# Kernel tuning notes

Measured on AMD Instinct MI355X. Metric: run time of the kernel, lower is better.

Reference implementation:

```python
import jax, jax.numpy as jnp
import numpy as np

S = 1    # support_num
K = 20   # KNN neighbor count for conv layers
B, V = 4, 4096


def _normalize(x, axis):
    n = jnp.linalg.norm(x, axis=axis, keepdims=True)
    return x / jnp.maximum(n, 1e-12)


def _knn(v, k):
    # v: (b, n, 3) -> (b, n, k) indices of k nearest (excluding self)
    sq = jnp.sum(v * v, axis=-1)
    dist = sq[:, :, None] + sq[:, None, :] - 2.0 * jnp.einsum('bic,bjc->bij', v, v)
    return jax.lax.top_k(-dist, k + 1)[1][:, :, 1:]


def _gather(feat, idx):
    # feat (b,n,c), idx (b,n,k) -> (b,n,k,c)
    return feat[jnp.arange(feat.shape[0])[:, None, None], idx]


def _dir_norm(verts, idx):
    nb = _gather(verts, idx)                       # (b,v,k,3)
    return _normalize(nb - verts[:, :, None, :], -1)


def _conv_surface(idx, verts, directions, kernel_num):
    b, v, k = idx.shape
    nd = _dir_norm(verts, idx)
    sd = _normalize(directions, 0)                 # (3, S*kernel_num)
    theta = jax.nn.relu(jnp.einsum('bvkc,cm->bvkm', nd, sd))
    theta = theta.reshape(b, v, k, S, kernel_num)
    return jnp.sum(jnp.max(theta, axis=2), axis=2)  # (b,v,kernel_num)


def _conv_layer(idx, verts, fm, W, bias, directions, out_c):
    b, v, k = idx.shape
    nd = _dir_norm(verts, idx)
    sd = _normalize(directions, 0)                 # (3, S*out_c)
    theta = jax.nn.relu(jnp.einsum('bvkc,cm->bvkm', nd, sd))  # (b,v,k,S*out_c)
    fo = fm @ W + bias                             # (b,v,(S+1)*out_c)
    center = fo[:, :, :out_c]
    support = _gather(fo[:, :, out_c:], idx)       # (b,v,k,S*out_c)
    act = (theta * support).reshape(b, v, k, S, out_c)
    return center + jnp.sum(jnp.max(act, axis=2), axis=2)


def _pool(verts, fm, rate, nn, seed):
    b, v, _ = verts.shape
    idx = _knn(verts, nn)
    pooled = jnp.max(_gather(fm, idx), axis=2)
    sel = jax.random.permutation(jax.random.key(seed), v)[: v // rate]
    return verts[:, sel, :], pooled[:, sel, :]


def _ln(x, g, b):
    m = jnp.mean(x, -1, keepdims=True)
    var = jnp.mean(jnp.square(x - m), -1, keepdims=True)
    return (x - m) / jnp.sqrt(var + 1e-6) * g + b


def _mha(q, kv, Win, bin_, Wout, bout, h):
    E = q.shape[-1]
    hd = E // h
    wq, wk, wv = jnp.split(Win, 3, axis=0)
    bq, bk, bv = jnp.split(bin_, 3)

    def heads(x, w, bb_):
        y = x @ w.T + bb_
        return y.reshape(y.shape[0], y.shape[1], h, hd).transpose(0, 2, 1, 3)

    qh, kh, vh = heads(q, wq, bq), heads(kv, wk, bk), heads(kv, wv, bv)
    a = jax.nn.softmax(jnp.einsum('bhqd,bhkd->bhqk', qh, kh) / jnp.sqrt(jnp.float32(hd)), -1)
    o = jnp.einsum('bhqk,bhkd->bhqd', a, vh).transpose(0, 2, 1, 3).reshape(q.shape)
    return o @ Wout.T + bout


def _conv1x1(x, W, b):
    # x (B,C,N,1) -> (B,O,N,1)
    return jnp.einsum('bcnl,oc->bonl', x, W) + b[None, :, None, None]


def _bn_train(x, g, b):
    # BatchNorm2d in training mode (batch statistics), eps=1e-5
    m = jnp.mean(x, axis=(0, 2, 3), keepdims=True)
    v = jnp.var(x, axis=(0, 2, 3), keepdims=True)
    return (x - m) / jnp.sqrt(v + 1e-5) * g[None, :, None, None] + b[None, :, None, None]


def _forward(vertices, d0, g0, be0, w1, b1, dir1, g1, be1, w2, b2, dir2, g2, be2,
             w3, b3, dir3, g3, be3, token, a1_in_w, a1_in_b, a1_out_w, a1_out_b,
             ffn1_w, ffn1_b, bg, bb, ffn2_w, ffn2_b, a2_in_w, a2_in_b, a2_out_w,
             a2_out_b, w7, b7, dir7, g4, be4, c8_w, c8_b):
    b = vertices.shape[0]
    v0 = vertices[:, 0]                                 # (b, 4096, 3)
    idx0 = _knn(v0, K)
    fm0 = jax.nn.relu(_ln(_conv_surface(idx0, v0, d0, 32), g0, be0))
    fm1 = jax.nn.relu(_ln(_conv_layer(idx0, v0, fm0, w1, b1, dir1, 64), g1, be1))
    v1, fm1 = _pool(v0, fm1, 4, 4, 1)                   # (b,1024,3), (b,1024,64)
    idx1 = _knn(v1, K)
    fm_x = fm1
    fm2 = jax.nn.relu(_ln(_conv_layer(idx1, v1, fm1, w2, b2, dir2, 128), g2, be2))
    fm3 = jax.nn.relu(_ln(_conv_layer(idx1, v1, fm2, w3, b3, dir3, 256), g3, be3))
    _, fm3 = _pool(v1, fm3, 4, 4, 2)                    # (b,256,256)
    tok = jnp.tile(token, (b, 1, 1, 1))[:, :, :, 0].transpose(0, 2, 1)  # (b,1024,64)
    query = _mha(tok, fm_x, a1_in_w, a1_in_b, a1_out_w, a1_out_b, 4) + fm_x
    q2 = query.transpose(0, 2, 1)[:, :, :, None]        # (b,64,1024,1)
    q2 = _conv1x1(jax.nn.relu(_bn_train(_conv1x1(q2, ffn1_w, ffn1_b), bg, bb)), ffn2_w, ffn2_b)
    query = q2[:, :, :, 0].transpose(0, 2, 1)           # (b,1024,256)
    cross = _mha(query, fm3, a2_in_w, a2_in_b, a2_out_w, a2_out_b, 4) + query
    fmf = jax.nn.relu(_ln(_conv_layer(idx1, v1, cross, w7, b7, dir7, 1024), g4, be4))
    fmf = fmf.transpose(0, 2, 1)[:, :, :, None]         # (b,1024,1024,1)
    return _conv1x1(fmf, c8_w, c8_b)                    # (b,256,1024,1)


def setup_inputs():
    ks = iter(jax.random.split(jax.random.key(0), 64))

    def rn(shape, s=0.05):
        return jax.random.normal(next(ks), shape, dtype=jnp.float32) * s

    f32 = jnp.float32
    return dict(
        vertices=jax.random.normal(next(ks), (B, 1, V, 3), dtype=f32),
        d0=rn((3, S * 32)), g0=jnp.ones((32,), f32), be0=jnp.zeros((32,), f32),
        w1=rn((32, (S + 1) * 64)), b1=rn(((S + 1) * 64,)), dir1=rn((3, S * 64)),
        g1=jnp.ones((64,), f32), be1=jnp.zeros((64,), f32),
        w2=rn((64, (S + 1) * 128)), b2=rn(((S + 1) * 128,)), dir2=rn((3, S * 128)),
        g2=jnp.ones((128,), f32), be2=jnp.zeros((128,), f32),
        w3=rn((128, (S + 1) * 256)), b3=rn(((S + 1) * 256,)), dir3=rn((3, S * 256)),
        g3=jnp.ones((256,), f32), be3=jnp.zeros((256,), f32),
        token=rn((1, 64, 1024, 1), 1.0),
        a1_in_w=rn((192, 64)), a1_in_b=rn((192,)), a1_out_w=rn((64, 64)), a1_out_b=rn((64,)),
        ffn1_w=rn((256, 64)), ffn1_b=rn((256,)), bg=jnp.ones((256,), f32), bb=jnp.zeros((256,), f32),
        ffn2_w=rn((256, 256)), ffn2_b=rn((256,)),
        a2_in_w=rn((768, 256)), a2_in_b=rn((768,)), a2_out_w=rn((256, 256)), a2_out_b=rn((256,)),
        w7=rn((256, (S + 1) * 1024)), b7=rn(((S + 1) * 1024,)), dir7=rn((3, S * 1024)),
        g4=jnp.ones((1024,), f32), be4=jnp.zeros((1024,), f32),
        c8_w=rn((256, 1024)), c8_b=rn((256,)),
    )


def reference(vertices, d0, g0, be0, w1, b1, dir1, g1, be1, w2, b2, dir2, g2, be2,
              w3, b3, dir3, g3, be3, token, a1_in_w, a1_in_b, a1_out_w, a1_out_b,
              ffn1_w, ffn1_b, bg, bb, ffn2_w, ffn2_b, a2_in_w, a2_in_b, a2_out_w,
              a2_out_b, w7, b7, dir7, g4, be4, c8_w, c8_b):
    return _forward(vertices, d0, g0, be0, w1, b1, dir1, g1, be1, w2, b2, dir2, g2,
                    be2, w3, b3, dir3, g3, be3, token, a1_in_w, a1_in_b, a1_out_w,
                    a1_out_b, ffn1_w, ffn1_b, bg, bb, ffn2_w, ffn2_b, a2_in_w,
                    a2_in_b, a2_out_w, a2_out_b, w7, b7, dir7, g4, be4, c8_w, c8_b)
```

## Files before the change

kernel.cpp:

```cpp
#include <hip/hip_runtime.h>
#include <stdint.h>
#include <stddef.h>

#define FINF __builtin_inff()

__device__ inline void tf2x32(uint32_t k0, uint32_t k1, uint32_t x0, uint32_t x1,
                              uint32_t* o0, uint32_t* o1) {
  uint32_t ks2 = k0 ^ k1 ^ 0x1BD11BDAu;
  uint32_t v0 = x0 + k0, v1 = x1 + k1;
#define TFR(r) { v0 += v1; v1 = (v1 << (r)) | (v1 >> (32 - (r))); v1 ^= v0; }
  TFR(13) TFR(15) TFR(26) TFR(6)
  v0 += k1;  v1 += ks2 + 1u;
  TFR(17) TFR(29) TFR(16) TFR(24)
  v0 += ks2; v1 += k0 + 2u;
  TFR(13) TFR(15) TFR(26) TFR(6)
  v0 += k0;  v1 += k1 + 3u;
  TFR(17) TFR(29) TFR(16) TFR(24)
  v0 += k1;  v1 += ks2 + 4u;
  TFR(13) TFR(15) TFR(26) TFR(6)
  v0 += ks2; v1 += k0 + 5u;
#undef TFR
  *o0 = v0; *o1 = v1;
}

__device__ inline void perm_subkey(uint32_t seed, int round, uint32_t* s0, uint32_t* s1) {
  uint32_t k0 = 0u, k1 = seed;
  for (int r = 0; r < round; r++) {
    uint32_t a0, a1; tf2x32(k0, k1, 0u, 0u, &a0, &a1);
    k0 = a0; k1 = a1;
  }
  tf2x32(k0, k1, 0u, 1u, s0, s1);
}

__global__ __launch_bounds__(256) void perm_pass_kernel(uint32_t seed, int round, int n,
                                                        const int* __restrict__ vin,
                                                        int* __restrict__ vout, int m) {
  __shared__ unsigned long long lk[4096];
  __shared__ int part[256];
  uint32_t s0, s1; perm_subkey(seed, round, &s0, &s1);
  int t = threadIdx.x;
  for (int j = t; j < n; j += 256) {
    uint32_t y0, y1; tf2x32(s0, s1, 0u, (uint32_t)j, &y0, &y1);
    lk[j] = ((unsigned long long)(y0 ^ y1) << 32) | (unsigned)j;
  }
  __syncthreads();
  int r = blockIdx.x * 64 + (t & 63);
  int q = t >> 6;
  unsigned long long ki = lk[r];
  int cnt = 0;
  int j0 = q * (n >> 2), j1 = j0 + (n >> 2);
  for (int j = j0; j < j1; j++) cnt += (lk[j] < ki) ? 1 : 0;
  part[t] = cnt;
  __syncthreads();
  if (t < 64) {
    int rank = part[t] + part[t + 64] + part[t + 128] + part[t + 192];
    if (rank < m) vout[rank] = vin ? vin[r] : r;
  }
}

__global__ __launch_bounds__(256) void perm_passA_kernel(int* __restrict__ pt1,
                                                         int* __restrict__ sel2) {
  __shared__ unsigned long long lk[4096];
  __shared__ int part[256];
  bool big = (blockIdx.x < 64);
  uint32_t seed = big ? 1u : 2u;
  int n = big ? 4096 : 1024;
  int m = big ? 4096 : 256;
  int* vout = big ? pt1 : sel2;
  int blk = big ? blockIdx.x : (blockIdx.x - 64);
  uint32_t s0, s1; perm_subkey(seed, 0, &s0, &s1);
  int t = threadIdx.x;
  for (int j = t; j < n; j += 256) {
    uint32_t y0, y1; tf2x32(s0, s1, 0u, (uint32_t)j, &y0, &y1);
    lk[j] = ((unsigned long long)(y0 ^ y1) << 32) | (unsigned)j;
  }
  __syncthreads();
  int r = blk * 64 + (t & 63);
  int q = t >> 6;
  unsigned long long ki = lk[r];
  int cnt = 0;
  int j0 = q * (n >> 2), j1 = j0 + (n >> 2);
  for (int j = j0; j < j1; j++) cnt += (lk[j] < ki) ? 1 : 0;
  part[t] = cnt;
  __syncthreads();
  if (t < 64) {
    int rank = part[t] + part[t + 64] + part[t + 128] + part[t + 192];
    if (rank < m) vout[rank] = r;
  }
}

__device__ inline void wave_argmin2(float head_d, int head_i, float* Mo, int* wio) {
  float M = head_d;
#pragma unroll
  for (int off = 1; off < 64; off <<= 1) M = fminf(M, __shfl_xor(M, off));
  int cand = (head_d == M) ? head_i : 0x7fffffff;
#pragma unroll
  for (int off = 1; off < 64; off <<= 1) cand = min(cand, __shfl_xor(cand, off));
  *Mo = M; *wio = cand;
}

template <int CNT, int WAVES>
__global__ __launch_bounds__(64 * WAVES) void knn_lex_kernel(const float* __restrict__ verts,
                                                             int N,
                                                             int* __restrict__ idx20,
                                                             int* __restrict__ idx4) {
  constexpr int SH = (CNT - 1 < 21) ? (CNT - 1) : 21;
  int row = blockIdx.x; int b = row / N, i = row - b * N;
  int t = threadIdx.x; int w = t >> 6; int lane = t & 63;
  const float* vb = verts + (size_t)b * N * 3;
  float xi = vb[i * 3], yi = vb[i * 3 + 1], zi = vb[i * 3 + 2];
  float sqi = (xi * xi + yi * yi) + zi * zi;

  int base = w * (N / WAVES) + lane;
  unsigned long long qe[CNT];
#pragma unroll
  for (int m = 0; m < CNT; m++) {
    int j = base + m * 64;
    float xj = vb[j * 3], yj = vb[j * 3 + 1], zj = vb[j * 3 + 2];
    float sqj = (xj * xj + yj * yj) + zj * zj;
    float dot = (xi * xj + yi * yj) + zi * zj;
    float d = sqi + sqj - 2.f * dot;
    qe[m] = ((unsigned long long)__float_as_uint(d) << 32) | (unsigned)j;
  }
#pragma unroll
  for (int k = 2; k <= CNT; k <<= 1)
#pragma unroll
    for (int j = k >> 1; j > 0; j >>= 1)
#pragma unroll
      for (int m = 0; m < CNT; m++) {
        int l = m ^ j;
        if (l > m) {
          unsigned long long a = qe[m], c = qe[l];
          bool up = ((m & k) == 0);
          bool sw = up ? (a > c) : (a < c);
          qe[m] = sw ? c : a;
          qe[l] = sw ? a : c;
        }
      }

  __shared__ float wd[WAVES][21];
  __shared__ int wi[WAVES][21];
  for (int r = 0; r < 21; r++) {
    float hd = __uint_as_float((uint32_t)(qe[0] >> 32));
    int hi = (int)(qe[0] & 0xffffffffu);
    float M; int widx;
    wave_argmin2(hd, hi, &M, &widx);
    if (lane == 0) { wd[w][r] = M; wi[w][r] = widx; }
    bool win = (hi == widx);
#pragma unroll
    for (int m = 0; m < SH; m++) qe[m] = win ? qe[m + 1] : qe[m];
    if (SH == CNT - 1) {
      if (win) qe[CNT - 1] = 0x7F8000007FFFFFFFull;
    }
  }
  __syncthreads();
  if (lane < 21) {
    float d0 = wd[w][lane]; int i0 = wi[w][lane];
    int rank = lane;
#pragma unroll
    for (int w2 = 0; w2 < WAVES; w2++) {
      if (w2 == w) continue;
      for (int p = 0; p < 21; p++) {
        float ld = wd[w2][p]; int li = wi[w2][p];
        rank += (ld < d0 || (ld == d0 && li < i0)) ? 1 : 0;
      }
    }
    if (rank >= 1 && rank <= 20) idx20[(size_t)row * 20 + (rank - 1)] = i0;
    if (rank >= 1 && rank <= 4)  idx4[(size_t)row * 4 + (rank - 1)] = i0;
  }
}

template <int CNT>
__global__ __launch_bounds__(64) void knn_1w_lex_kernel(const float* __restrict__ verts, int N,
                                                        int* __restrict__ idx20,
                                                        int* __restrict__ idx4) {
  int row = blockIdx.x; int b = row / N, i = row - b * N;
  int lane = threadIdx.x;
  const float* vb = verts + (size_t)b * N * 3;
  float xi = vb[i * 3], yi = vb[i * 3 + 1], zi = vb[i * 3 + 2];
  float sqi = (xi * xi + yi * yi) + zi * zi;

  unsigned long long qe[CNT];
#pragma unroll
  for (int m = 0; m < CNT; m++) {
    int j = lane + m * 64;
    float xj = vb[j * 3], yj = vb[j * 3 + 1], zj = vb[j * 3 + 2];
    float sqj = (xj * xj + yj * yj) + zj * zj;
    float dot = (xi * xj + yi * yj) + zi * zj;
    float d = sqi + sqj - 2.f * dot;
    qe[m] = ((unsigned long long)__float_as_uint(d) << 32) | (unsigned)j;
  }
#pragma unroll
  for (int k = 2; k <= CNT; k <<= 1)
#pragma unroll
    for (int j = k >> 1; j > 0; j >>= 1)
#pragma unroll
      for (int m = 0; m < CNT; m++) {
        int l = m ^ j;
        if (l > m) {
          unsigned long long a = qe[m], c = qe[l];
          bool up = ((m & k) == 0);
          bool sw = up ? (a > c) : (a < c);
          qe[m] = sw ? c : a;
          qe[l] = sw ? a : c;
        }
      }
  for (int r = 0; r < 21; r++) {
    float hd = __uint_as_float((uint32_t)(qe[0] >> 32));
    int hi = (int)(qe[0] & 0xffffffffu);
    float M; int widx;
    wave_argmin2(hd, hi, &M, &widx);
    if (lane == 0 && r >= 1) {
      idx20[(size_t)row * 20 + (r - 1)] = widx;
      if (r <= 4) idx4[(size_t)row * 4 + (r - 1)] = widx;
    }
    bool win = (hi == widx);
#pragma unroll
    for (int m = 0; m < CNT - 1; m++) qe[m] = win ? qe[m + 1] : qe[m];
    if (win) qe[CNT - 1] = 0x7F8000007FFFFFFFull;
  }
}

__global__ void conv_surface_kernel(const float* __restrict__ verts,
                                    const int* __restrict__ idx20,
                                    const float* __restrict__ d0,
                                    const float* __restrict__ g, const float* __restrict__ be,
                                    float* __restrict__ out, int N) {
  int row = blockIdx.x; int b = row / N, i = row - b * N;
  int t = threadIdx.x;
  __shared__ float nd[20][3];
  const float* vb = verts + (size_t)b * N * 3;
  if (t < 20) {
    int j = idx20[(size_t)row * 20 + t];
    float dx = vb[j * 3] - vb[i * 3], dy = vb[j * 3 + 1] - vb[i * 3 + 1], dz = vb[j * 3 + 2] - vb[i * 3 + 2];
    float n2 = sqrtf(dx * dx + dy * dy + dz * dz); n2 = fmaxf(n2, 1e-12f);
    nd[t][0] = dx / n2; nd[t][1] = dy / n2; nd[t][2] = dz / n2;
  }
  __syncthreads();
  float x = 0.f;
  if (t < 32) {
    float a = d0[t], bb2 = d0[32 + t], c = d0[64 + t];
    float nrm = fmaxf(sqrtf(a * a + bb2 * bb2 + c * c), 1e-12f);
    a /= nrm; bb2 /= nrm; c /= nrm;
    float mx = -FINF;
    for (int kk = 0; kk < 20; kk++) {
      float th = fmaxf(nd[kk][0] * a + nd[kk][1] * bb2 + nd[kk][2] * c, 0.f);
      mx = fmaxf(mx, th);
    }
    x = mx;
  }
  float s = x;
  for (int off = 32; off; off >>= 1) s += __shfl_xor(s, off);
  float mean = s / 32.f;
  float dev = (t < 32) ? x - mean : 0.f;
  float s2 = dev * dev;
  for (int off = 32; off; off >>= 1) s2 += __shfl_xor(s2, off);
  float var = s2 / 32.f;
  if (t < 32) {
    float y = (x - mean) / sqrtf(var + 1e-6f) * g[t] + be[t];
    out[(size_t)row * 32 + t] = fmaxf(y, 0.f);
  }
}

__global__ void gemm_io_kernel(const float* __restrict__ x, const float* __restrict__ W,
                               const float* __restrict__ bias, float* __restrict__ y,
                               int R, int I, int O) {
  int rb = blockIdx.x * 8;
  int o = blockIdx.y * blockDim.x + threadIdx.x;
  __shared__ float xs[256][8];
  for (int u = 0; u < 8; u++)
    for (int i2 = threadIdx.x; i2 < I; i2 += blockDim.x) xs[i2][u] = x[(size_t)(rb + u) * I + i2];
  __syncthreads();
  float a[8] = {0, 0, 0, 0, 0, 0, 0, 0};
  for (int k2 = 0; k2 < I; k2++) {
    float wv = W[(size_t)k2 * O + o];
    float4 xa = *(const float4*)&xs[k2][0];
    float4 xb = *(const float4*)&xs[k2][4];
    a[0] += xa.x * wv; a[1] += xa.y * wv; a[2] += xa.z * wv; a[3] += xa.w * wv;
    a[4] += xb.x * wv; a[5] += xb.y * wv; a[6] += xb.z * wv; a[7] += xb.w * wv;
  }
  float bv = bias[o];
#pragma unroll
  for (int u = 0; u < 8; u++) y[(size_t)(rb + u) * O + o] = a[u] + bv;
}

__global__ void gemm_io16_kernel(const float* __restrict__ x, const float* __restrict__ W,
                                 const float* __restrict__ bias, float* __restrict__ y,
                                 int R, int I, int O) {
  int rb = blockIdx.x * 16;
  int o = blockIdx.y * blockDim.x + threadIdx.x;
  __shared__ float xs[256][16];
  for (int u = 0; u < 16; u++)
    for (int i2 = threadIdx.x; i2 < I; i2 += blockDim.x) xs[i2][u] = x[(size_t)(rb + u) * I + i2];
  __syncthreads();
  float a[16];
#pragma unroll
  for (int u = 0; u < 16; u++) a[u] = 0.f;
  for (int k2 = 0; k2 < I; k2++) {
    float wv = W[(size_t)k2 * O + o];
    float4 x0 = *(const float4*)&xs[k2][0];
    float4 x1 = *(const float4*)&xs[k2][4];
    float4 x2 = *(const float4*)&xs[k2][8];
    float4 x3 = *(const float4*)&xs[k2][12];
    a[0] += x0.x * wv; a[1] += x0.y * wv; a[2] += x0.z * wv; a[3] += x0.w * wv;
    a[4] += x1.x * wv; a[5] += x1.y * wv; a[6] += x1.z * wv; a[7] += x1.w * wv;
    a[8] += x2.x * wv; a[9] += x2.y * wv; a[10] += x2.z * wv; a[11] += x2.w * wv;
    a[12] += x3.x * wv; a[13] += x3.y * wv; a[14] += x3.z * wv; a[15] += x3.w * wv;
  }
  float bv = bias[o];
#pragma unroll
  for (int u = 0; u < 16; u++) y[(size_t)(rb + u) * O + o] = a[u] + bv;
}

template <int CPT>
__global__ void combine_kernel(const float* __restrict__ verts, const int* __restrict__ idx20,
                               const float* __restrict__ fo, const float* __restrict__ dirs,
                               const float* __restrict__ g, const float* __restrict__ be,
                               float* __restrict__ out, int N, int C) {
  int row = blockIdx.x; int b = row / N, i = row - b * N;
  int t = threadIdx.x, bs = blockDim.x;
  __shared__ float nd[20][3];
  __shared__ int nidx[20];
  __shared__ float red[8];
  const float* vb = verts + (size_t)b * N * 3;
  if (t < 20) {
    int j = idx20[(size_t)row * 20 + t];
    nidx[t] = j;
    float dx = vb[j * 3] - vb[i * 3], dy = vb[j * 3 + 1] - vb[i * 3 + 1], dz = vb[j * 3 + 2] - vb[i * 3 + 2];
    float n2 = fmaxf(sqrtf(dx * dx + dy * dy + dz * dz), 1e-12f);
    nd[t][0] = dx / n2; nd[t][1] = dy / n2; nd[t][2] = dz / n2;
  }
  __syncthreads();
  const float* fob = fo + (size_t)b * N * 2 * C;
  const float* forow = fob + (size_t)i * 2 * C;
  float da[CPT], db[CPT], dc[CPT], mx[CPT];
#pragma unroll
  for (int u = 0; u < CPT; u++) {
    int c = t + u * bs;
    float a = dirs[c], bb = dirs[C + c], cc = dirs[2 * C + c];
    float nrm = fmaxf(sqrtf(a * a + bb * bb + cc * cc), 1e-12f);
    da[u] = a / nrm; db[u] = bb / nrm; dc[u] = cc / nrm;
    mx[u] = -FINF;
  }
  for (int kk = 0; kk < 20; kk++) {
    float n0 = nd[kk][0], n1 = nd[kk][1], n2v = nd[kk][2];
    const float* sup = fob + (size_t)nidx[kk] * 2 * C + C + t;
#pragma unroll
    for (int u = 0; u < CPT; u++) {
      float th = fmaxf(n0 * da[u] + n1 * db[u] + n2v * dc[u], 0.f);
      mx[u] = fmaxf(mx[u], th * sup[u * bs]);
    }
  }
  float xv[CPT];
  float ssum = 0.f;
#pragma unroll
  for (int u = 0; u < CPT; u++) {
    int c = t + u * bs;
    float val = forow[c] + mx[u];
    xv[u] = val; ssum += val;
  }
  int nw = bs >> 6;
  for (int off = 32; off; off >>= 1) ssum += __shfl_down(ssum, off);
  if ((t & 63) == 0) red[t >> 6] = ssum;
  __syncthreads();
  if (t == 0) { float s = red[0]; for (int w = 1; w < nw; w++) s += red[w]; red[0] = s; }
  __syncthreads();
  float mean = red[0] / (float)C;
  __syncthreads();
  float s2 = 0.f;
#pragma unroll
  for (int u = 0; u < CPT; u++) { float d2 = xv[u] - mean; s2 += d2 * d2; }
  for (int off = 32; off; off >>= 1) s2 += __shfl_down(s2, off);
  if ((t & 63) == 0) red[t >> 6] = s2;
  __syncthreads();
  if (t == 0) { float s = red[0]; for (int w = 1; w < nw; w++) s += red[w]; red[0] = s; }
  __syncthreads();
  float inv = 1.0f / sqrtf(red[0] / (float)C + 1e-6f);
#pragma unroll
  for (int u = 0; u < CPT; u++) {
    int c = t + u * bs;
    float yv = (xv[u] - mean) * inv * g[c] + be[c];
    out[(size_t)row * C + c] = fmaxf(yv, 0.f);
  }
}

__global__ void pool_select_kernel(const float* __restrict__ fm, const int* __restrict__ idx4,
                                   const int* __restrict__ sel, const float* __restrict__ vin,
                                   float* __restrict__ vout, float* __restrict__ out,
                                   int N, int M, int C) {
  int row = blockIdx.x; int b = row / M, r = row - b * M;
  int s = sel[r];
  const int* id = idx4 + ((size_t)b * N + s) * 4;
  int i0 = id[0], i1 = id[1], i2 = id[2], i3 = id[3];
  const float* fb = fm + (size_t)b * N * C;
  for (int c = threadIdx.x; c < C; c += blockDim.x) {
    float m = fmaxf(fmaxf(fb[(size_t)i0 * C + c], fb[(size_t)i1 * C + c]),
                    fmaxf(fb[(size_t)i2 * C + c], fb[(size_t)i3 * C + c]));
    out[((size_t)b * M + r) * C + c] = m;
  }
  if (vout != nullptr && threadIdx.x < 3)
    vout[((size_t)b * M + r) * 3 + threadIdx.x] = vin[((size_t)b * N + s) * 3 + threadIdx.x];
}

__global__ void linear_oi_kernel(const float* __restrict__ x, const float* __restrict__ W,
                                 const float* __restrict__ bias, const float* __restrict__ res,
                                 float* __restrict__ y, int R, int I, int O) {
  int rb = blockIdx.x * 8;
  int o = threadIdx.x;
  __shared__ float xs[8][256];
  for (int u = 0; u < 8; u++)
    for (int i2 = threadIdx.x; i2 < I; i2 += O) xs[u][i2] = x[(size_t)(rb + u) * I + i2];
  __syncthreads();
  float a[8] = {0, 0, 0, 0, 0, 0, 0, 0};
  const float* w = W + (size_t)o * I;
  for (int k2 = 0; k2 < I; k2++) {
    float wv = w[k2];
#pragma unroll
    for (int u = 0; u < 8; u++) a[u] += xs[u][k2] * wv;
  }
  float bv = bias[o];
#pragma unroll
  for (int u = 0; u < 8; u++) {
    float val = a[u] + bv;
    if (res) val += res[(size_t)(rb + u) * O + o];
    y[(size_t)(rb + u) * O + o] = val;
  }
}

__global__ __launch_bounds__(64) void qkv1_kernel(const float* __restrict__ token,
                                                  const float* __restrict__ fm1p,
                                                  const float* __restrict__ Win,
                                                  const float* __restrict__ bin,
                                                  float* __restrict__ Q1,
                                                  float* __restrict__ K1,
                                                  float* __restrict__ V1) {
  int ybr = blockIdx.y;
  const float* W = Win + (size_t)ybr * 64 * 64;
  const float* bias = bin + ybr * 64;
  float* out = (ybr == 0) ? Q1 : (ybr == 1) ? K1 : V1;
  int rb = blockIdx.x * 8;
  int o = threadIdx.x;
  __shared__ float xs[8][64];
  if (ybr == 0) {
    for (int u = 0; u < 8; u++) {
      int n = (rb + u) & 1023;
      xs[u][o] = token[(size_t)o * 1024 + n];
    }
  } else {
    for (int u = 0; u < 8; u++) xs[u][o] = fm1p[(size_t)(rb + u) * 64 + o];
  }
  __syncthreads();
  float a[8] = {0, 0, 0, 0, 0, 0, 0, 0};
  const float* w = W + (size_t)o * 64;
  for (int k2 = 0; k2 < 64; k2++) {
    float wv = w[k2];
#pragma unroll
    for (int u = 0; u < 8; u++) a[u] += xs[u][k2] * wv;
  }
  float bv = bias[o];
#pragma unroll
  for (int u = 0; u < 8; u++) out[(size_t)(rb + u) * 64 + o] = a[u] + bv;
}

__global__ __launch_bounds__(256) void kv2_kernel(const float* __restrict__ fm3p,
                                                  const float* __restrict__ Win,
                                                  const float* __restrict__ bin,
                                                  float* __restrict__ K2,
                                                  float* __restrict__ V2) {
  int ybr = blockIdx.y;
  const float* W = Win + (size_t)(1 + ybr) * 256 * 256;
  const float* bias = bin + (1 + ybr) * 256;
  float* out = ybr ? V2 : K2;
  int rb = blockIdx.x * 8;
  int o = threadIdx.x;
  __shared__ float xs[8][256];
  for (int u = 0; u < 8; u++) xs[u][o] = fm3p[(size_t)(rb + u) * 256 + o];
  __syncthreads();
  float a[8] = {0, 0, 0, 0, 0, 0, 0, 0};
  const float* w = W + (size_t)o * 256;
  for (int k2 = 0; k2 < 256; k2++) {
    float wv = w[k2];
#pragma unroll
    for (int u = 0; u < 8; u++) a[u] += xs[u][k2] * wv;
  }
  float bv = bias[o];
#pragma unroll
  for (int u = 0; u < 8; u++) out[(size_t)(rb + u) * 256 + o] = a[u] + bv;
}

template <int HD, int QPT, int KS>
__global__ __launch_bounds__(256) void attn_tiled(
    const float* __restrict__ q, const float* __restrict__ kk,
    const float* __restrict__ vv, float* __restrict__ o,
    int Lq, int Lk, int H, float scale) {
  constexpr int TK = 64;
  constexpr int QG = 256 / (2 * KS);
  constexpr int QPB = QG * QPT;
  constexpr int V4 = HD / 4;
  constexpr int STR = V4 + 1;
  constexpr int HH = HD / 2;
  constexpr int V4H = HH / 4;

  __shared__ float4 Ks[TK * STR];
  __shared__ float4 Vs[TK * STR];

  int t = threadIdx.x;
  int dh = t & 1;
  int ki = (t >> 1) & (KS - 1);
  int qg = t / (2 * KS);
  int nqt = Lq / QPB;
  int qt = blockIdx.x % nqt, bh = blockIdx.x / nqt;
  int h = bh % H, b = bh / H;
  int E = H * HD;
  int q0 = qt * QPB + qg * QPT;

  const float* qbase = q + ((size_t)b * Lq + q0) * E + h * HD + dh * HH;
  const float* kbase = kk + (size_t)b * Lk * E + h * HD;
  const float* vbase = vv + (size_t)b * Lk * E + h * HD;

  float qr[QPT][HH], O[QPT][HH], m[QPT], l[QPT];
#pragma unroll
  for (int r = 0; r < QPT; r++) {
    m[r] = -FINF; l[r] = 0.f;
#pragma unroll
    for (int d = 0; d < HH; d++) { qr[r][d] = qbase[(size_t)r * E + d]; O[r][d] = 0.f; }
  }

  for (int k0 = 0; k0 < Lk; k0 += TK) {
    __syncthreads();
    for (int e = t; e < TK * V4; e += 256) {
      int rr = e / V4, cc = e - rr * V4;
      Ks[rr * STR + cc] = *(const float4*)(kbase + (size_t)(k0 + rr) * E + cc * 4);
      Vs[rr * STR + cc] = *(const float4*)(vbase + (size_t)(k0 + rr) * E + cc * 4);
    }
    __syncthreads();
#pragma unroll 1
    for (int g = 0; g < TK / KS; g += 4) {
      float sc[QPT][4];
#pragma unroll
      for (int jj = 0; jj < 4; jj++) {
        int kl = (g + jj) * KS + ki;
        float sh[QPT];
#pragma unroll
        for (int r = 0; r < QPT; r++) sh[r] = 0.f;
        const float4* kr = &Ks[kl * STR + dh * V4H];
#pragma unroll
        for (int c = 0; c < V4H; c++) {
          float4 kv = kr[c];
#pragma unroll
          for (int r = 0; r < QPT; r++)
            sh[r] += qr[r][4 * c] * kv.x + qr[r][4 * c + 1] * kv.y
                   + qr[r][4 * c + 2] * kv.z + qr[r][4 * c + 3] * kv.w;
        }
#pragma unroll
        for (int r = 0; r < QPT; r++)
          sc[r][jj] = (sh[r] + __shfl_xor(sh[r], 1)) * scale;
      }
#pragma unroll
      for (int r = 0; r < QPT; r++) {
        float tm = fmaxf(fmaxf(sc[r][0], sc[r][1]), fmaxf(sc[r][2], sc[r][3]));
        float nm = fmaxf(m[r], tm);
        float a = __expf(m[r] - nm);
        m[r] = nm;
        float ls = l[r] * a;
#pragma unroll
        for (int d = 0; d < HH; d++) O[r][d] *= a;
#pragma unroll
        for (int jj = 0; jj < 4; jj++) { sc[r][jj] = __expf(sc[r][jj] - nm); ls += sc[r][jj]; }
        l[r] = ls;
      }
#pragma unroll
      for (int jj = 0; jj < 4; jj++) {
        int kl = (g + jj) * KS + ki;
        const float4* vr = &Vs[kl * STR + dh * V4H];
#pragma unroll
        for (int c = 0; c < V4H; c++) {
          float4 v4 = vr[c];
#pragma unroll
          for (int r = 0; r < QPT; r++) {
            O[r][4 * c]     += sc[r][jj] * v4.x;
            O[r][4 * c + 1] += sc[r][jj] * v4.y;
            O[r][4 * c + 2] += sc[r][jj] * v4.z;
            O[r][4 * c + 3] += sc[r][jj] * v4.w;
          }
        }
      }
    }
  }
#pragma unroll
  for (int r = 0; r < QPT; r++) {
    float M = m[r];
#pragma unroll
    for (int mask = 2; mask < 2 * KS; mask <<= 1) M = fmaxf(M, __shfl_xor(M, mask));
    float w = __expf(m[r] - M);
    float ll = l[r] * w;
#pragma unroll
    for (int mask = 2; mask < 2 * KS; mask <<= 1) ll += __shfl_xor(ll, mask);
    float inv = 1.f / ll;
#pragma unroll
    for (int d = 0; d < HH; d++) {
      float x = O[r][d] * w;
#pragma unroll
      for (int mask = 2; mask < 2 * KS; mask <<= 1) x += __shfl_xor(x, mask);
      O[r][d] = x * inv;
    }
  }
  if (ki == 0) {
    float* obase = o + ((size_t)b * Lq + q0) * E + h * HD + dh * HH;
#pragma unroll
    for (int r = 0; r < QPT; r++)
#pragma unroll
      for (int d = 0; d < HH; d++) obase[(size_t)r * E + d] = O[r][d];
  }
}

__global__ void bn_stats_kernel(const float* __restrict__ x, float* __restrict__ stats,
                                int R, int C) {
  int c = blockIdx.x; int t = threadIdx.x;
  __shared__ float red[8];
  float s = 0.f;
  for (int r = t; r < R; r += blockDim.x) s += x[(size_t)r * C + c];
  for (int off = 32; off; off >>= 1) s += __shfl_down(s, off);
  if ((t & 63) == 0) red[t >> 6] = s;
  __syncthreads();
  if (t == 0) { float a = red[0]; for (int w = 1; w < (int)(blockDim.x >> 6); w++) a += red[w]; red[0] = a; }
  __syncthreads();
  float mean = red[0] / (float)R;
  __syncthreads();
  float s2 = 0.f;
  for (int r = t; r < R; r += blockDim.x) { float d = x[(size_t)r * C + c] - mean; s2 += d * d; }
  for (int off = 32; off; off >>= 1) s2 += __shfl_down(s2, off);
  if ((t & 63) == 0) red[t >> 6] = s2;
  __syncthreads();
  if (t == 0) {
    float a = red[0]; for (int w = 1; w < (int)(blockDim.x >> 6); w++) a += red[w];
    stats[c] = mean; stats[C + c] = a / (float)R;
  }
}

__global__ void bn_apply_kernel(float* __restrict__ x, const float* __restrict__ stats,
                                const float* __restrict__ g, const float* __restrict__ b2,
                                int total, int C) {
  int id = blockIdx.x * blockDim.x + threadIdx.x;
  if (id >= total) return;
  int c = id % C;
  float y = (x[id] - stats[c]) / sqrtf(stats[C + c] + 1e-5f) * g[c] + b2[c];
  x[id] = fmaxf(y, 0.f);
}

__global__ void final_kernel(const float* __restrict__ fmf, const float* __restrict__ W,
                             const float* __restrict__ bias, float* __restrict__ out) {
  int nb = blockIdx.x * 8;
  int o = threadIdx.x;
  __shared__ float xs[1024][8];
  for (int u = 0; u < 8; u++)
    for (int c = threadIdx.x; c < 1024; c += 256) xs[c][u] = fmf[(size_t)(nb + u) * 1024 + c];
  __syncthreads();
  float acc[8] = {0, 0, 0, 0, 0, 0, 0, 0};
  const float* w = W + (size_t)o * 1024;
  for (int c = 0; c < 1024; c++) {
    float wv = w[c];
    float4 xa = *(const float4*)&xs[c][0];
    float4 xb = *(const float4*)&xs[c][4];
    acc[0] += xa.x * wv; acc[1] += xa.y * wv; acc[2] += xa.z * wv; acc[3] += xa.w * wv;
    acc[4] += xb.x * wv; acc[5] += xb.y * wv; acc[6] += xb.z * wv; acc[7] += xb.w * wv;
  }
  float bv = bias[o];
#pragma unroll
  for (int u = 0; u < 8; u++) {
    int r = nb + u; int b = r >> 10; int n = r & 1023;
    out[((size_t)(b * 256 + o) << 10) + n] = acc[u] + bv;
  }
}

extern "C" void kernel_launch(void* const* d_in, const int* in_sizes, int n_in,
                              void* d_out, int out_size, void* d_ws, size_t ws_size,
                              hipStream_t stream) {
  (void)in_sizes; (void)n_in; (void)out_size;
  const float* vertices = (const float*)d_in[0];
  const float* d0       = (const float*)d_in[1];
  const float* g0       = (const float*)d_in[2];
  const float* be0      = (const float*)d_in[3];
  const float* w1       = (const float*)d_in[4];
  const float* b1       = (const float*)d_in[5];
  const float* dir1     = (const float*)d_in[6];
  const float* g1       = (const float*)d_in[7];
  const float* be1      = (const float*)d_in[8];
  const float* w2       = (const float*)d_in[9];
  const float* b2       = (const float*)d_in[10];
  const float* dir2     = (const float*)d_in[11];
  const float* g2       = (const float*)d_in[12];
  const float* be2      = (const float*)d_in[13];
  const float* w3       = (const float*)d_in[14];
  const float* b3       = (const float*)d_in[15];
  const float* dir3     = (const float*)d_in[16];
  const float* g3       = (const float*)d_in[17];
  const float* be3      = (const float*)d_in[18];
  const float* token    = (const float*)d_in[19];
  const float* a1_in_w  = (const float*)d_in[20];
  const float* a1_in_b  = (const float*)d_in[21];
  const float* a1_out_w = (const float*)d_in[22];
  const float* a1_out_b = (const float*)d_in[23];
  const float* ffn1_w   = (const float*)d_in[24];
  const float* ffn1_b   = (const float*)d_in[25];
  const float* bg       = (const float*)d_in[26];
  const float* bbp      = (const float*)d_in[27];
  const float* ffn2_w   = (const float*)d_in[28];
  const float* ffn2_b   = (const float*)d_in[29];
  const float* a2_in_w  = (const float*)d_in[30];
  const float* a2_in_b  = (const float*)d_in[31];
  const float* a2_out_w = (const float*)d_in[32];
  const float* a2_out_b = (const float*)d_in[33];
  const float* w7       = (const float*)d_in[34];
  const float* b7       = (const float*)d_in[35];
  const float* dir7     = (const float*)d_in[36];
  const float* g4       = (const float*)d_in[37];
  const float* be4      = (const float*)d_in[38];
  const float* c8_w     = (const float*)d_in[39];
  const float* c8_b     = (const float*)d_in[40];
  float* out = (float*)d_out;
  float* ws = (float*)d_ws;

  if (ws_size < 78568448u) return;

  float* FO     = ws + 0;
  float* S1     = ws + 8388608;
  float* S2     = ws + 12582912;
  float* S3     = ws + 13631488;
  float* QUERY2 = ws + 14680064;
  float* CROSS  = ws + 15728640;
  float* FM1P   = ws + 16777216;
  float* FM3P   = FM1P + 262144;
  float* TOK    = FM3P + 262144;
  float* Q1     = TOK + 262144;
  float* K1     = Q1 + 262144;
  float* VA1    = K1 + 262144;
  float* ATT1   = VA1 + 262144;
  float* K2     = ATT1 + 262144;
  float* V2     = K2 + 262144;
  float* V1     = V2 + 262144;
  float* BNST   = V1 + 12288;
  int* IDX20_0  = (int*)(BNST + 512);
  int* IDX4_0   = IDX20_0 + 327680;
  int* IDX20_1  = IDX4_0 + 65536;
  int* IDX4_1   = IDX20_1 + 81920;
  int* SEL1     = IDX4_1 + 16384;
  int* SEL2     = SEL1 + 1024;
  int* PT1 = IDX20_0;

  perm_passA_kernel<<<80, 256, 0, stream>>>(PT1, SEL2);
  perm_pass_kernel<<<64, 256, 0, stream>>>(1u, 1, 4096, PT1, SEL1, 1024);

  knn_lex_kernel<32, 2><<<4 * 4096, 128, 0, stream>>>(vertices, 4096, IDX20_0, IDX4_0);
  conv_surface_kernel<<<4 * 4096, 64, 0, stream>>>(vertices, IDX20_0, d0, g0, be0, S2, 4096);
  gemm_io_kernel<<<dim3(2048, 1), 128, 0, stream>>>(S2, w1, b1, FO, 16384, 32, 128);
  combine_kernel<1><<<16384, 64, 0, stream>>>(vertices, IDX20_0, FO, dir1, g1, be1, S1, 4096, 64);
  pool_select_kernel<<<4096, 64, 0, stream>>>(S1, IDX4_0, SEL1, vertices, V1, FM1P, 4096, 1024, 64);

  knn_1w_lex_kernel<16><<<4 * 1024, 64, 0, stream>>>(V1, 1024, IDX20_1, IDX4_1);
  gemm_io_kernel<<<dim3(512, 1), 256, 0, stream>>>(FM1P, w2, b2, FO, 4096, 64, 256);
  combine_kernel<1><<<4096, 128, 0, stream>>>(V1, IDX20_1, FO, dir2, g2, be2, S2, 1024, 128);
  gemm_io_kernel<<<dim3(512, 2), 256, 0, stream>>>(S2, w3, b3, FO, 4096, 128, 512);
  combine_kernel<1><<<4096, 256, 0, stream>>>(V1, IDX20_1, FO, dir3, g3, be3, S3, 1024, 256);
  pool_select_kernel<<<1024, 256, 0, stream>>>(S3, IDX4_1, SEL2, nullptr, nullptr, FM3P, 1024, 256, 256);

  qkv1_kernel<<<dim3(512, 3), 64, 0, stream>>>(token, FM1P, a1_in_w, a1_in_b, Q1, K1, VA1);
  attn_tiled<16, 2, 8><<<512, 256, 0, stream>>>(Q1, K1, VA1, ATT1, 1024, 1024, 4, 0.25f);
  linear_oi_kernel<<<512, 64, 0, stream>>>(ATT1, a1_out_w, a1_out_b, FM1P, S3, 4096, 64, 64);

  linear_oi_kernel<<<512, 256, 0, stream>>>(S3, ffn1_w, ffn1_b, nullptr, S2, 4096, 64, 256);
  bn_stats_kernel<<<256, 256, 0, stream>>>(S2, BNST, 4096, 256);
  bn_apply_kernel<<<4096, 256, 0, stream>>>(S2, BNST, bg, bbp, 4096 * 256, 256);
  linear_oi_kernel<<<512, 256, 0, stream>>>(S2, ffn2_w, ffn2_b, nullptr, QUERY2, 4096, 256, 256);

  linear_oi_kernel<<<512, 256, 0, stream>>>(QUERY2, a2_in_w, a2_in_b, nullptr, S3, 4096, 256, 256);
  kv2_kernel<<<dim3(128, 2), 256, 0, stream>>>(FM3P, a2_in_w, a2_in_b, K2, V2);
  attn_tiled<64, 2, 8><<<512, 256, 0, stream>>>(S3, K2, V2, S1, 1024, 256, 4, 0.125f);
  linear_oi_kernel<<<512, 256, 0, stream>>>(S1, a2_out_w, a2_out_b, QUERY2, CROSS, 4096, 256, 256);

  gemm_io16_kernel<<<dim3(256, 8), 256, 0, stream>>>(CROSS, w7, b7, FO, 4096, 256, 2048);
  combine_kernel<4><<<4096, 256, 0, stream>>>(V1, IDX20_1, FO, dir7, g4, be4, S1, 1024, 1024);
  final_kernel<<<512, 256, 0, stream>>>(S1, c8_w, c8_b, out);
}
```

Baseline: 934.4 us.

## Split KNN sort keys, fuse BN into linear, merge KNN with GEMM, pack conv_surface

The KNN bitonic sort now keeps separate float distance and int index arrays instead of packed 64-bit keys. The second-level KNN is packed four rows per 256-thread block and launched in the same grid as the w2 GEMM. conv_surface runs four rows per block and drops the block barrier, since each wave only reads its own slice. Batch-norm apply is folded into the loading stage of the ffn2 linear kernel, removing a full read-modify-write pass and one launch. Together these cut launch count and per-block overhead. The cost is a different tie-break path in the sort, and the new layout for the embedded GEMM weights must match the original gemm_io_kernel.

```diff
diff --git a/kernel.cpp b/kernel.cpp
--- a/kernel.cpp
+++ b/kernel.cpp
@@ -112,15 +112,15 @@
   float sqi = (xi * xi + yi * yi) + zi * zi;
 
   int base = w * (N / WAVES) + lane;
-  unsigned long long qe[CNT];
+  float qd[CNT]; int qi[CNT];
 #pragma unroll
   for (int m = 0; m < CNT; m++) {
     int j = base + m * 64;
     float xj = vb[j * 3], yj = vb[j * 3 + 1], zj = vb[j * 3 + 2];
     float sqj = (xj * xj + yj * yj) + zj * zj;
     float dot = (xi * xj + yi * yj) + zi * zj;
-    float d = sqi + sqj - 2.f * dot;
-    qe[m] = ((unsigned long long)__float_as_uint(d) << 32) | (unsigned)j;
+    qd[m] = sqi + sqj - 2.f * dot;
+    qi[m] = j;
   }
 #pragma unroll
   for (int k = 2; k <= CNT; k <<= 1)
@@ -130,27 +130,27 @@
       for (int m = 0; m < CNT; m++) {
         int l = m ^ j;
         if (l > m) {
-          unsigned long long a = qe[m], c = qe[l];
           bool up = ((m & k) == 0);
-          bool sw = up ? (a > c) : (a < c);
-          qe[m] = sw ? c : a;
-          qe[l] = sw ? a : c;
+          bool sw = up ? (qd[m] > qd[l]) : (qd[m] < qd[l]);
+          float td = sw ? qd[l] : qd[m]; qd[l] = sw ? qd[m] : qd[l]; qd[m] = td;
+          int ti = sw ? qi[l] : qi[m]; qi[l] = sw ? qi[m] : qi[l]; qi[m] = ti;
         }
       }
 
   __shared__ float wd[WAVES][21];
   __shared__ int wi[WAVES][21];
   for (int r = 0; r < 21; r++) {
-    float hd = __uint_as_float((uint32_t)(qe[0] >> 32));
-    int hi = (int)(qe[0] & 0xffffffffu);
     float M; int widx;
-    wave_argmin2(hd, hi, &M, &widx);
+    wave_argmin2(qd[0], qi[0], &M, &widx);
     if (lane == 0) { wd[w][r] = M; wi[w][r] = widx; }
-    bool win = (hi == widx);
-#pragma unroll
-    for (int m = 0; m < SH; m++) qe[m] = win ? qe[m + 1] : qe[m];
+    bool win = (qi[0] == widx);
+#pragma unroll
+    for (int m = 0; m < SH; m++) {
+      qd[m] = win ? qd[m + 1] : qd[m];
+      qi[m] = win ? qi[m + 1] : qi[m];
+    }
     if (SH == CNT - 1) {
-      if (win) qe[CNT - 1] = 0x7F8000007FFFFFFFull;
+      if (win) { qd[CNT - 1] = FINF; qi[CNT - 1] = 0x7fffffff; }
     }
   }
   __syncthreads();
@@ -170,73 +170,99 @@
   }
 }
 
-template <int CNT>
-__global__ __launch_bounds__(64) void knn_1w_lex_kernel(const float* __restrict__ verts, int N,
-                                                        int* __restrict__ idx20,
-                                                        int* __restrict__ idx4) {
-  int row = blockIdx.x; int b = row / N, i = row - b * N;
-  int lane = threadIdx.x;
-  const float* vb = verts + (size_t)b * N * 3;
-  float xi = vb[i * 3], yi = vb[i * 3 + 1], zi = vb[i * 3 + 2];
-  float sqi = (xi * xi + yi * yi) + zi * zi;
-
-  unsigned long long qe[CNT];
-#pragma unroll
-  for (int m = 0; m < CNT; m++) {
-    int j = lane + m * 64;
-    float xj = vb[j * 3], yj = vb[j * 3 + 1], zj = vb[j * 3 + 2];
-    float sqj = (xj * xj + yj * yj) + zj * zj;
-    float dot = (xi * xj + yi * yj) + zi * zj;
-    float d = sqi + sqj - 2.f * dot;
-    qe[m] = ((unsigned long long)__float_as_uint(d) << 32) | (unsigned)j;
-  }
-#pragma unroll
-  for (int k = 2; k <= CNT; k <<= 1)
-#pragma unroll
-    for (int j = k >> 1; j > 0; j >>= 1)
-#pragma unroll
-      for (int m = 0; m < CNT; m++) {
-        int l = m ^ j;
-        if (l > m) {
-          unsigned long long a = qe[m], c = qe[l];
-          bool up = ((m & k) == 0);
-          bool sw = up ? (a > c) : (a < c);
-          qe[m] = sw ? c : a;
-          qe[l] = sw ? a : c;
+__global__ __launch_bounds__(256) void knnv1_w2_kernel(const float* __restrict__ verts,
+                                                       int* __restrict__ idx20,
+                                                       int* __restrict__ idx4,
+                                                       const float* __restrict__ x,
+                                                       const float* __restrict__ W,
+                                                       const float* __restrict__ bias,
+                                                       float* __restrict__ y) {
+  if (blockIdx.x < 1024) {
+    constexpr int CNT = 16;
+    const int N = 1024;
+    int lane = threadIdx.x & 63;
+    int row = blockIdx.x * 4 + (threadIdx.x >> 6);
+    int b = row / N, i = row - b * N;
+    const float* vb = verts + (size_t)b * N * 3;
+    float xi = vb[i * 3], yi = vb[i * 3 + 1], zi = vb[i * 3 + 2];
+    float sqi = (xi * xi + yi * yi) + zi * zi;
+    float qd[CNT]; int qi[CNT];
+#pragma unroll
+    for (int m = 0; m < CNT; m++) {
+      int j = lane + m * 64;
+      float xj = vb[j * 3], yj = vb[j * 3 + 1], zj = vb[j * 3 + 2];
+      float sqj = (xj * xj + yj * yj) + zj * zj;
+      float dot = (xi * xj + yi * yj) + zi * zj;
+      qd[m] = sqi + sqj - 2.f * dot;
+      qi[m] = j;
+    }
+#pragma unroll
+    for (int k = 2; k <= CNT; k <<= 1)
+#pragma unroll
+      for (int j = k >> 1; j > 0; j >>= 1)
+#pragma unroll
+        for (int m = 0; m < CNT; m++) {
+          int l = m ^ j;
+          if (l > m) {
+            bool up = ((m & k) == 0);
+            bool sw = up ? (qd[m] > qd[l]) : (qd[m] < qd[l]);
+            float td = sw ? qd[l] : qd[m]; qd[l] = sw ? qd[m] : qd[l]; qd[m] = td;
+            int ti = sw ? qi[l] : qi[m]; qi[l] = sw ? qi[m] : qi[l]; qi[m] = ti;
+          }
         }
+    for (int r = 0; r < 21; r++) {
+      float M; int widx;
+      wave_argmin2(qd[0], qi[0], &M, &widx);
+      if (lane == 0 && r >= 1) {
+        idx20[(size_t)row * 20 + (r - 1)] = widx;
+        if (r <= 4) idx4[(size_t)row * 4 + (r - 1)] = widx;
       }
-  for (int r = 0; r < 21; r++) {
-    float hd = __uint_as_float((uint32_t)(qe[0] >> 32));
-    int hi = (int)(qe[0] & 0xffffffffu);
-    float M; int widx;
-    wave_argmin2(hd, hi, &M, &widx);
-    if (lane == 0 && r >= 1) {
-      idx20[(size_t)row * 20 + (r - 1)] = widx;
-      if (r <= 4) idx4[(size_t)row * 4 + (r - 1)] = widx;
-    }
-    bool win = (hi == widx);
-#pragma unroll
-    for (int m = 0; m < CNT - 1; m++) qe[m] = win ? qe[m + 1] : qe[m];
-    if (win) qe[CNT - 1] = 0x7F8000007FFFFFFFull;
-  }
-}
-
-__global__ void conv_surface_kernel(const float* __restrict__ verts,
-                                    const int* __restrict__ idx20,
-                                    const float* __restrict__ d0,
-                                    const float* __restrict__ g, const float* __restrict__ be,
-                                    float* __restrict__ out, int N) {
-  int row = blockIdx.x; int b = row / N, i = row - b * N;
-  int t = threadIdx.x;
-  __shared__ float nd[20][3];
+      bool win = (qi[0] == widx);
+#pragma unroll
+      for (int m = 0; m < CNT - 1; m++) {
+        qd[m] = win ? qd[m + 1] : qd[m];
+        qi[m] = win ? qi[m + 1] : qi[m];
+      }
+      if (win) { qd[CNT - 1] = FINF; qi[CNT - 1] = 0x7fffffff; }
+    }
+  } else {
+    const int I = 64, O = 256;
+    int rb = (blockIdx.x - 1024) * 8;
+    int o = threadIdx.x;
+    __shared__ float xs[64][8];
+    for (int u = 0; u < 8; u++)
+      for (int i2 = threadIdx.x; i2 < I; i2 += 256) xs[i2][u] = x[(size_t)(rb + u) * I + i2];
+    __syncthreads();
+    float a[8] = {0, 0, 0, 0, 0, 0, 0, 0};
+    for (int k2 = 0; k2 < I; k2++) {
+      float wv = W[(size_t)k2 * O + o];
+      float4 xa = *(const float4*)&xs[k2][0];
+      float4 xb = *(const float4*)&xs[k2][4];
+      a[0] += xa.x * wv; a[1] += xa.y * wv; a[2] += xa.z * wv; a[3] += xa.w * wv;
+      a[4] += xb.x * wv; a[5] += xb.y * wv; a[6] += xb.z * wv; a[7] += xb.w * wv;
+    }
+    float bv = bias[o];
+#pragma unroll
+    for (int u = 0; u < 8; u++) y[(size_t)(rb + u) * O + o] = a[u] + bv;
+  }
+}
+
+__global__ __launch_bounds__(256) void conv_surface_kernel(const float* __restrict__ verts,
+                                                           const int* __restrict__ idx20,
+                                                           const float* __restrict__ d0,
+                                                           const float* __restrict__ g,
+                                                           const float* __restrict__ be,
+                                                           float* __restrict__ out, int N) {
+  int w = threadIdx.x >> 6; int t = threadIdx.x & 63;
+  int row = blockIdx.x * 4 + w; int b = row / N, i = row - b * N;
+  __shared__ float nd[4][20][3];
   const float* vb = verts + (size_t)b * N * 3;
   if (t < 20) {
     int j = idx20[(size_t)row * 20 + t];
     float dx = vb[j * 3] - vb[i * 3], dy = vb[j * 3 + 1] - vb[i * 3 + 1], dz = vb[j * 3 + 2] - vb[i * 3 + 2];
     float n2 = sqrtf(dx * dx + dy * dy + dz * dz); n2 = fmaxf(n2, 1e-12f);
-    nd[t][0] = dx / n2; nd[t][1] = dy / n2; nd[t][2] = dz / n2;
-  }
-  __syncthreads();
+    nd[w][t][0] = dx / n2; nd[w][t][1] = dy / n2; nd[w][t][2] = dz / n2;
+  }
   float x = 0.f;
   if (t < 32) {
     float a = d0[t], bb2 = d0[32 + t], c = d0[64 + t];
@@ -244,7 +270,7 @@
     a /= nrm; bb2 /= nrm; c /= nrm;
     float mx = -FINF;
     for (int kk = 0; kk < 20; kk++) {
-      float th = fmaxf(nd[kk][0] * a + nd[kk][1] * bb2 + nd[kk][2] * c, 0.f);
+      float th = fmaxf(nd[w][kk][0] * a + nd[w][kk][1] * bb2 + nd[w][kk][2] * c, 0.f);
       mx = fmaxf(mx, th);
     }
     x = mx;
@@ -425,6 +451,33 @@
     if (res) val += res[(size_t)(rb + u) * O + o];
     y[(size_t)(rb + u) * O + o] = val;
   }
+}
+
+__global__ void linear_bn_kernel(const float* __restrict__ x, const float* __restrict__ W,
+                                 const float* __restrict__ bias,
+                                 const float* __restrict__ stats,
+                                 const float* __restrict__ g, const float* __restrict__ b2,
+                                 float* __restrict__ y, int R, int I, int O) {
+  int rb = blockIdx.x * 8;
+  int o = threadIdx.x;
+  __shared__ float xs[8][256];
+  for (int u = 0; u < 8; u++)
+    for (int i2 = threadIdx.x; i2 < I; i2 += O) {
+      float xr = x[(size_t)(rb + u) * I + i2];
+      float yv = (xr - stats[i2]) / sqrtf(stats[I + i2] + 1e-5f) * g[i2] + b2[i2];
+      xs[u][i2] = fmaxf(yv, 0.f);
+    }
+  __syncthreads();
+  float a[8] = {0, 0, 0, 0, 0, 0, 0, 0};
+  const float* w = W + (size_t)o * I;
+  for (int k2 = 0; k2 < I; k2++) {
+    float wv = w[k2];
+#pragma unroll
+    for (int u = 0; u < 8; u++) a[u] += xs[u][k2] * wv;
+  }
+  float bv = bias[o];
+#pragma unroll
+  for (int u = 0; u < 8; u++) y[(size_t)(rb + u) * O + o] = a[u] + bv;
 }
 
 __global__ __launch_bounds__(64) void qkv1_kernel(const float* __restrict__ token,
@@ -636,16 +689,6 @@
     float a = red[0]; for (int w = 1; w < (int)(blockDim.x >> 6); w++) a += red[w];
     stats[c] = mean; stats[C + c] = a / (float)R;
   }
-}
-
-__global__ void bn_apply_kernel(float* __restrict__ x, const float* __restrict__ stats,
-                                const float* __restrict__ g, const float* __restrict__ b2,
-                                int total, int C) {
-  int id = blockIdx.x * blockDim.x + threadIdx.x;
-  if (id >= total) return;
-  int c = id % C;
-  float y = (x[id] - stats[c]) / sqrtf(stats[C + c] + 1e-5f) * g[c] + b2[c];
-  x[id] = fmaxf(y, 0.f);
 }
 
 __global__ void final_kernel(const float* __restrict__ fmf, const float* __restrict__ W,
@@ -752,13 +795,12 @@
   perm_pass_kernel<<<64, 256, 0, stream>>>(1u, 1, 4096, PT1, SEL1, 1024);
 
   knn_lex_kernel<32, 2><<<4 * 4096, 128, 0, stream>>>(vertices, 4096, IDX20_0, IDX4_0);
-  conv_surface_kernel<<<4 * 4096, 64, 0, stream>>>(vertices, IDX20_0, d0, g0, be0, S2, 4096);
+  conv_surface_kernel<<<4096, 256, 0, stream>>>(vertices, IDX20_0, d0, g0, be0, S2, 4096);
   gemm_io_kernel<<<dim3(2048, 1), 128, 0, stream>>>(S2, w1, b1, FO, 16384, 32, 128);
   combine_kernel<1><<<16384, 64, 0, stream>>>(vertices, IDX20_0, FO, dir1, g1, be1, S1, 4096, 64);
   pool_select_kernel<<<4096, 64, 0, stream>>>(S1, IDX4_0, SEL1, vertices, V1, FM1P, 4096, 1024, 64);
 
-  knn_1w_lex_kernel<16><<<4 * 1024, 64, 0, stream>>>(V1, 1024, IDX20_1, IDX4_1);
-  gemm_io_kernel<<<dim3(512, 1), 256, 0, stream>>>(FM1P, w2, b2, FO, 4096, 64, 256);
+  knnv1_w2_kernel<<<1536, 256, 0, stream>>>(V1, IDX20_1, IDX4_1, FM1P, w2, b2, FO);
   combine_kernel<1><<<4096, 128, 0, stream>>>(V1, IDX20_1, FO, dir2, g2, be2, S2, 1024, 128);
   gemm_io_kernel<<<dim3(512, 2), 256, 0, stream>>>(S2, w3, b3, FO, 4096, 128, 512);
   combine_kernel<1><<<4096, 256, 0, stream>>>(V1, IDX20_1, FO, dir3, g3, be3, S3, 1024, 256);
@@ -770,8 +812,7 @@
 
   linear_oi_kernel<<<512, 256, 0, stream>>>(S3, ffn1_w, ffn1_b, nullptr, S2, 4096, 64, 256);
   bn_stats_kernel<<<256, 256, 0, stream>>>(S2, BNST, 4096, 256);
-  bn_apply_kernel<<<4096, 256, 0, stream>>>(S2, BNST, bg, bbp, 4096 * 256, 256);
-  linear_oi_kernel<<<512, 256, 0, stream>>>(S2, ffn2_w, ffn2_b, nullptr, QUERY2, 4096, 256, 256);
+  linear_bn_kernel<<<512, 256, 0, stream>>>(S2, ffn2_w, ffn2_b, BNST, bg, bbp, QUERY2, 4096, 256, 256);
 
   linear_oi_kernel<<<512, 256, 0, stream>>>(QUERY2, a2_in_w, a2_in_b, nullptr, S3, 4096, 256, 256);
   kv2_kernel<<<dim3(128, 2), 256, 0, stream>>>(FM3P, a2_in_w, a2_in_b, K2, V2);
```

Measured after the change: 910.7 us. 2.5% less time.
